# Kernel tuning notes

Hardware: AMD Instinct MI355X
Metric: run time of the kernel (lower is better)

The kernel has to match this reference:

```python
import jax, jax.numpy as jnp
import numpy as np

N = 50000      # num nodes
E = 800000     # num edges (avg degree 16)
D_IN = 128     # input feature dim
H = 128        # hidden dim
RD = 32        # relation embedding dim
L = 2          # num layers
R = 16         # num relations


def setup_inputs() -> dict:
    key = jax.random.key(0)
    ks = jax.random.split(key, 16)
    f32 = jnp.float32
    def lin(k, out_d, in_d):
        return jax.random.normal(k, (out_d, in_d), dtype=f32) * (1.0 / np.sqrt(in_d))
    return {
        "x": jax.random.normal(ks[0], (N, D_IN), dtype=f32),
        "in_W": lin(ks[1], H, D_IN),
        "in_b": jnp.zeros((H,), f32),
        # per-layer stacked params [L, ...]
        "rel_emb": jax.random.normal(ks[2], (L, R, RD), dtype=f32) * 0.02,
        "msg_W": jax.random.normal(ks[3], (L, H, H + RD), dtype=f32) * (1.0 / np.sqrt(H + RD)),
        "msg_b": jnp.zeros((L, H), f32),
        "self_W": jax.random.normal(ks[4], (L, H, H), dtype=f32) * (1.0 / np.sqrt(H)),
        "self_b": jnp.zeros((L, H), f32),
        "neigh_W": jax.random.normal(ks[5], (L, H, H), dtype=f32) * (1.0 / np.sqrt(H)),
        "neigh_b": jnp.zeros((L, H), f32),
        "edge_src": jax.random.randint(ks[6], (E,), 0, N),
        "edge_dst": jax.random.randint(ks[7], (E,), 0, N),
        "rel_ids": jax.random.randint(ks[8], (E,), 0, R),
    }


def reference(x, in_W, in_b, rel_emb, msg_W, msg_b, self_W, self_b,
              neigh_W, neigh_b, edge_src, edge_dst, rel_ids):
    # input projection (dropout is identity at eval)
    h = x @ in_W.T + in_b
    ones_e = jnp.ones((edge_dst.shape[0], 1), h.dtype)
    deg = jax.ops.segment_sum(ones_e, edge_dst, num_segments=N)   # [N,1]
    deg = jnp.maximum(deg, 1.0)
    for l in range(L):
        rel = rel_emb[l][rel_ids]                                  # [E,RD] gather
        msg_in = jnp.concatenate([h[edge_src], rel], axis=-1)      # [E,H+RD]
        msg = msg_in @ msg_W[l].T + msg_b[l]                       # [E,H]
        agg = jax.ops.segment_sum(msg, edge_dst, num_segments=N) / deg  # mean agg
        h = jax.nn.relu(h @ self_W[l].T + self_b[l] + agg @ neigh_W[l].T + neigh_b[l])
    return h
```

## Files before the change

### kernel.cpp

```cpp
#include <hip/hip_runtime.h>
#include <hip/hip_bf16.h>

#define NN 50000
#define EE 800000
#define DH 128
#define RDIM 32
#define RR 16
#define HRD 160
#define HSW 384
#define SCAN_B ((NN + 255) / 256)

typedef __attribute__((ext_vector_type(8))) short bf16x8;
typedef __attribute__((ext_vector_type(4))) float f32x4;

__device__ __forceinline__ ushort f2b(float v) {
    uint u = __float_as_uint(v);
    return (ushort)((u + 0x7fffu + ((u >> 16) & 1u)) >> 16);
}
__device__ __forceinline__ float b2f(ushort b) { return __uint_as_float(((uint)b) << 16); }

__global__ __launch_bounds__(256) void k_count(const int* __restrict__ dst,
                                               int* deg, int* ord) {
    int e = blockIdx.x * 256 + threadIdx.x;
    if (e < EE) ord[e] = atomicAdd(&deg[dst[e]], 1);
}

__global__ __launch_bounds__(256) void k_scan_part(const int* __restrict__ deg,
                                                   int* rp, int* bsum) {
    __shared__ int s[256];
    int tid = threadIdx.x;
    int i = blockIdx.x * 256 + tid;
    int v = (i < NN) ? deg[i] : 0;
    s[tid] = v;
    __syncthreads();
    for (int off = 1; off < 256; off <<= 1) {
        int t = (tid >= off) ? s[tid - off] : 0;
        __syncthreads();
        s[tid] += t;
        __syncthreads();
    }
    if (i < NN) rp[i] = s[tid] - v;
    if (tid == 255) bsum[blockIdx.x] = s[255];
}

__global__ __launch_bounds__(256) void k_scan_bsum(const int* __restrict__ bsum, int* boff) {
    __shared__ int s[256];
    int tid = threadIdx.x;
    int v = (tid < SCAN_B) ? bsum[tid] : 0;
    s[tid] = v;
    __syncthreads();
    for (int off = 1; off < 256; off <<= 1) {
        int t = (tid >= off) ? s[tid - off] : 0;
        __syncthreads();
        s[tid] += t;
        __syncthreads();
    }
    boff[tid] = s[tid] - v;
}

__global__ __launch_bounds__(256) void k_scan_add(const int* __restrict__ boff, int* rp) {
    int i = blockIdx.x * 256 + threadIdx.x;
    if (i < NN) rp[i] += boff[blockIdx.x];
    if (i == 0) rp[NN] = EE;
}

__global__ __launch_bounds__(256) void k_fill(const int* __restrict__ src,
                                              const int* __restrict__ dst,
                                              const int* __restrict__ rel,
                                              const int* __restrict__ ord,
                                              const int* __restrict__ rp,
                                              int* __restrict__ col) {
    int e = blockIdx.x * 256 + threadIdx.x;
    if (e < EE) {
        int p = rp[dst[e]] + ord[e];
        col[p] = src[e] | (rel[e] << 16);
    }
}


__global__ __launch_bounds__(256) void k_prep_inWb(const float* __restrict__ w,
                                                   ushort* __restrict__ o) {
    int i = blockIdx.x * 256 + threadIdx.x;
    o[i] = f2b(w[i]);
}

__global__ __launch_bounds__(256) void k_prep_msgWb(const float* __restrict__ msgW,
                                                    const float* __restrict__ relE,
                                                    ushort* __restrict__ B1,
                                                    float* __restrict__ RMf32) {
    int t = threadIdx.x;
    int l = t >> 7, f = t & 127;
    const float* mw = msgW + (size_t)l * DH * HRD + f * HRD;
    ushort* out = B1 + ((size_t)l * DH + f) * DH;
    for (int k = 0; k < DH; ++k) out[k] = f2b(mw[k]);
    for (int r = 0; r < RR; ++r) {
        float acc = 0.f;
        for (int c = 0; c < RDIM; ++c)
            acc += relE[l * RR * RDIM + r * RDIM + c] * mw[DH + c];
        RMf32[(size_t)l * RR * DH + r * DH + f] = acc;
    }
}

__global__ __launch_bounds__(256) void k_prep_wc2b(const float* __restrict__ selfW,
                                                   const float* __restrict__ neighW,
                                                   ushort* __restrict__ o) {
    int idx = blockIdx.x * 256 + threadIdx.x;
    int l = idx >> 15, rem = idx & 32767;
    int f = rem >> 8, k = rem & 255;
    float v = (k < DH) ? selfW[(size_t)l * DH * DH + f * DH + k]
                       : neighW[(size_t)l * DH * DH + f * DH + (k - DH)];
    o[idx] = f2b(v);
}

__global__ __launch_bounds__(256) void k_seg(ushort* __restrict__ hs,
                                             const int* __restrict__ rp,
                                             const int* __restrict__ col,
                                             const float* __restrict__ RM) {
    __shared__ float RM_s[RR * DH];
    int t = threadIdx.x;
    for (int i = t; i < RR * DH; i += 256) RM_s[i] = RM[i];
    __syncthreads();
    int wid = t >> 6, lane = t & 63;
    int n = blockIdx.x * 4 + wid;
    if (n >= NN) return;
    int beg = rp[n], end = rp[n + 1];
    float ax = 0.f, ay = 0.f, rx = 0.f, ry = 0.f;
    const float* rm0 = RM_s + lane * 2;
    for (int j0 = beg; j0 < end; j0 += 64) {
        int myc = (j0 + lane < end) ? col[j0 + lane] : 0;
        int m = min(64, end - j0);
        for (int jj = 0; jj < m; ++jj) {
            int packed = __shfl(myc, jj, 64);
            int sidx = packed & 0xffff;
            int rel = packed >> 16;
            uint v = *(const uint*)(hs + (size_t)sidx * HSW + lane * 2);
            ax += b2f((ushort)(v & 0xffffu));
            ay += b2f((ushort)(v >> 16));
            rx += rm0[rel * DH];
            ry += rm0[rel * DH + 1];
        }
    }
    uint ps = ((uint)f2b(ay) << 16) | (uint)f2b(ax);
    uint pr = ((uint)f2b(ry) << 16) | (uint)f2b(rx);
    *(uint*)(hs + (size_t)n * HSW + 128 + lane * 2) = ps;
    *(uint*)(hs + (size_t)n * HSW + 256 + lane * 2) = pr;
}

template <int K, int EPI, int AMODE>
__global__ __launch_bounds__(256) void k_mm(const void* __restrict__ Araw,
                                            const ushort* __restrict__ B,
                                            const float* __restrict__ bias1,
                                            const float* __restrict__ bias2,
                                            const int* __restrict__ deg,
                                            ushort* __restrict__ hs,
                                            float* __restrict__ outf) {
    constexpr int KC = (K == 256) ? 128 : K;
    constexpr int NCH = K / KC;
    constexpr int KP = KC + 8;
    __shared__ ushort A_s[64][KP];
    __shared__ ushort B_s[128][KP];
    __shared__ int deg_s[64];
    int t = threadIdx.x;
    int n0 = blockIdx.x * 64;
    int lane = t & 63, wid = t >> 6;
    int wm = wid >> 1, wn = wid & 1;

    if (EPI == 1 && t < 64) {
        int node = n0 + t;
        deg_s[t] = (node < NN) ? deg[node] : 1;
    }

    f32x4 acc[2][4];
    #pragma unroll
    for (int mt = 0; mt < 2; ++mt)
        #pragma unroll
        for (int nt = 0; nt < 4; ++nt) acc[mt][nt] = (f32x4)0.0f;

    for (int ch = 0; ch < NCH; ++ch) {
        int kc0 = ch * KC;
        if (AMODE == 0) {
            const float4* x4 = (const float4*)Araw;
            for (int idx = t; idx < 64 * (KC / 4); idx += 256) {
                int r = idx / (KC / 4), c = idx % (KC / 4);
                int node = min(n0 + r, NN - 1);
                float4 v = x4[(size_t)node * 32 + c];
                ushort* dstp = &A_s[r][c * 4];
                dstp[0] = f2b(v.x); dstp[1] = f2b(v.y);
                dstp[2] = f2b(v.z); dstp[3] = f2b(v.w);
            }
        } else {
            const ushort* Ab = (const ushort*)Araw;
            for (int idx = t; idx < 64 * (KC / 8); idx += 256) {
                int r = idx / (KC / 8), c = idx % (KC / 8);
                int node = min(n0 + r, NN - 1);
                *(uint4*)&A_s[r][c * 8] =
                    *(const uint4*)(Ab + (size_t)node * HSW + kc0 + c * 8);
            }
        }
        for (int idx = t; idx < 128 * (KC / 8); idx += 256) {
            int r = idx / (KC / 8), c = idx % (KC / 8);
            *(uint4*)&B_s[r][c * 8] =
                *(const uint4*)(B + (size_t)r * K + kc0 + c * 8);
        }
        __syncthreads();

        #pragma unroll
        for (int ks = 0; ks < KC / 32; ++ks) {
            int k0 = ks * 32 + (lane >> 4) * 8;
            bf16x8 af[2], bfr[4];
            #pragma unroll
            for (int mt = 0; mt < 2; ++mt)
                af[mt] = *(const bf16x8*)&A_s[wm * 32 + mt * 16 + (lane & 15)][k0];
            #pragma unroll
            for (int nt = 0; nt < 4; ++nt)
                bfr[nt] = *(const bf16x8*)&B_s[wn * 64 + nt * 16 + (lane & 15)][k0];
            #pragma unroll
            for (int mt = 0; mt < 2; ++mt)
                #pragma unroll
                for (int nt = 0; nt < 4; ++nt)
                    acc[mt][nt] = __builtin_amdgcn_mfma_f32_16x16x32_bf16(
                        af[mt], bfr[nt], acc[mt][nt], 0, 0, 0);
        }
        if (ch + 1 < NCH) __syncthreads();
    }

    int fbase = wn * 64;
    #pragma unroll
    for (int mt = 0; mt < 2; ++mt) {
        #pragma unroll
        for (int rg = 0; rg < 4; ++rg) {
            int nl = wm * 32 + mt * 16 + ((lane >> 4) << 2) + rg;
            int node = n0 + nl;
            if (node >= NN) continue;
            #pragma unroll
            for (int nt = 0; nt < 4; ++nt) {
                int f = fbase + nt * 16 + (lane & 15);
                float v = acc[mt][nt][rg];
                if (EPI == 0) {
                    hs[(size_t)node * HSW + f] = f2b(v + bias1[f]);
                } else if (EPI == 1) {
                    int d = deg_s[nl];
                    float rmacc = b2f(hs[(size_t)node * HSW + 256 + f]);
                    float o = (v + rmacc) * (1.f / (float)max(d, 1))
                              + ((d > 0) ? bias1[f] : 0.f);
                    hs[(size_t)node * HSW + 128 + f] = f2b(o);
                } else {
                    float o = fmaxf(v + bias1[f] + bias2[f], 0.f);
                    if (EPI == 2) hs[(size_t)node * HSW + f] = f2b(o);
                    else          outf[(size_t)node * DH + f] = o;
                }
            }
        }
    }
}

extern "C" void kernel_launch(void* const* d_in, const int* in_sizes, int n_in,
                              void* d_out, int out_size, void* d_ws, size_t ws_size,
                              hipStream_t stream) {
    const float* x      = (const float*)d_in[0];
    const float* in_W   = (const float*)d_in[1];
    const float* in_b   = (const float*)d_in[2];
    const float* rel_e  = (const float*)d_in[3];
    const float* msg_W  = (const float*)d_in[4];
    const float* msg_b  = (const float*)d_in[5];
    const float* self_W = (const float*)d_in[6];
    const float* self_b = (const float*)d_in[7];
    const float* neigh_W= (const float*)d_in[8];
    const float* neigh_b= (const float*)d_in[9];
    const int* e_src    = (const int*)d_in[10];
    const int* e_dst    = (const int*)d_in[11];
    const int* r_ids    = (const int*)d_in[12];

    char* ws = (char*)d_ws;
    size_t off = 0;
    ushort* HS   = (ushort*)(ws + off); off += (size_t)NN * HSW * 2;
    ushort* inWb = (ushort*)(ws + off); off += (size_t)DH * DH * 2;
    ushort* B1   = (ushort*)(ws + off); off += 2 * (size_t)DH * DH * 2;
    ushort* Wc2b = (ushort*)(ws + off); off += 2 * (size_t)DH * 256 * 2;
    float*  RMf  = (float*)(ws + off);  off += 2 * (size_t)RR * DH * 4;
    int* deg  = (int*)(ws + off);
    int* rp   = deg + NN;
    int* bsum = rp + NN + 1;
    int* boff = bsum + 256;
    int* ord  = boff + 256;
    int* col  = ord + EE;

    hipMemsetAsync(deg, 0, sizeof(int) * NN, stream);

    k_count<<<(EE + 255) / 256, 256, 0, stream>>>(e_dst, deg, ord);
    k_scan_part<<<SCAN_B, 256, 0, stream>>>(deg, rp, bsum);
    k_scan_bsum<<<1, 256, 0, stream>>>(bsum, boff);
    k_scan_add<<<SCAN_B, 256, 0, stream>>>(boff, rp);
    k_fill<<<(EE + 255) / 256, 256, 0, stream>>>(e_src, e_dst, r_ids, ord, rp, col);

    k_prep_inWb<<<64, 256, 0, stream>>>(in_W, inWb);
    k_prep_msgWb<<<1, 256, 0, stream>>>(msg_W, rel_e, B1, RMf);
    k_prep_wc2b<<<256, 256, 0, stream>>>(self_W, neigh_W, Wc2b);

    const int GB = (NN + 63) / 64;
    k_mm<128, 0, 0><<<GB, 256, 0, stream>>>(x, inWb, in_b, nullptr, nullptr, HS, nullptr);

    for (int l = 0; l < 2; ++l) {
        k_seg<<<(NN + 3) / 4, 256, 0, stream>>>(HS, rp, col, RMf + (size_t)l * RR * DH);
        k_mm<128, 1, 1><<<GB, 256, 0, stream>>>(HS + 128, B1 + (size_t)l * DH * DH,
                                                msg_b + l * DH, nullptr, deg, HS, nullptr);
        if (l == 0)
            k_mm<256, 2, 1><<<GB, 256, 0, stream>>>(HS, Wc2b, self_b, neigh_b,
                                                    nullptr, HS, nullptr);
        else
            k_mm<256, 3, 1><<<GB, 256, 0, stream>>>(HS, Wc2b + (size_t)DH * 256,
                                                    self_b + DH, neigh_b + DH,
                                                    nullptr, HS, (float*)d_out);
    }
}
```

Before: 395.3 us.

## Process four edges per wave in segment aggregation with 16-byte row loads

The segment-sum kernel now splits each 64-lane wave into four groups of 16 lanes. Each group handles a different edge and loads a 16-byte chunk of the bf16 source row instead of a 4-byte pair per lane. Partial sums are combined across the groups with xor shuffles, and only the first group writes the result. The relation-message table is transposed to a [feature][relation] layout so each lane can index it with a stride. The intent is more memory-level parallelism and wider loads in the gather-bound aggregation. The cost is more registers and extra shuffle reductions, and the transposed table may cause LDS bank conflicts.

Measured after the change: 501.3 us. 1.27x slower.

```diff
diff --git a/kernel.cpp b/kernel.cpp
--- a/kernel.cpp
+++ b/kernel.cpp
@@ -77,7 +77,6 @@
     }
 }
 
-
 __global__ __launch_bounds__(256) void k_prep_inWb(const float* __restrict__ w,
                                                    ushort* __restrict__ o) {
     int i = blockIdx.x * 256 + threadIdx.x;
@@ -87,7 +86,7 @@
 __global__ __launch_bounds__(256) void k_prep_msgWb(const float* __restrict__ msgW,
                                                     const float* __restrict__ relE,
                                                     ushort* __restrict__ B1,
-                                                    float* __restrict__ RMf32) {
+                                                    float* __restrict__ RMt) {
     int t = threadIdx.x;
     int l = t >> 7, f = t & 127;
     const float* mw = msgW + (size_t)l * DH * HRD + f * HRD;
@@ -97,7 +96,7 @@
         float acc = 0.f;
         for (int c = 0; c < RDIM; ++c)
             acc += relE[l * RR * RDIM + r * RDIM + c] * mw[DH + c];
-        RMf32[(size_t)l * RR * DH + r * DH + f] = acc;
+        RMt[(size_t)l * DH * RR + f * RR + r] = acc;
     }
 }
 
@@ -115,35 +114,56 @@
 __global__ __launch_bounds__(256) void k_seg(ushort* __restrict__ hs,
                                              const int* __restrict__ rp,
                                              const int* __restrict__ col,
-                                             const float* __restrict__ RM) {
-    __shared__ float RM_s[RR * DH];
+                                             const float* __restrict__ RMt) {
+    __shared__ float RM_s[DH * RR];
     int t = threadIdx.x;
-    for (int i = t; i < RR * DH; i += 256) RM_s[i] = RM[i];
+    for (int i = t; i < DH * RR; i += 256) RM_s[i] = RMt[i];
     __syncthreads();
     int wid = t >> 6, lane = t & 63;
     int n = blockIdx.x * 4 + wid;
     if (n >= NN) return;
     int beg = rp[n], end = rp[n + 1];
-    float ax = 0.f, ay = 0.f, rx = 0.f, ry = 0.f;
-    const float* rm0 = RM_s + lane * 2;
+    int q = lane >> 4, r = lane & 15;
+    float a[8], rm[8];
+    #pragma unroll
+    for (int i = 0; i < 8; ++i) { a[i] = 0.f; rm[i] = 0.f; }
     for (int j0 = beg; j0 < end; j0 += 64) {
         int myc = (j0 + lane < end) ? col[j0 + lane] : 0;
-        int m = min(64, end - j0);
-        for (int jj = 0; jj < m; ++jj) {
-            int packed = __shfl(myc, jj, 64);
-            int sidx = packed & 0xffff;
-            int rel = packed >> 16;
-            uint v = *(const uint*)(hs + (size_t)sidx * HSW + lane * 2);
-            ax += b2f((ushort)(v & 0xffffu));
-            ay += b2f((ushort)(v >> 16));
-            rx += rm0[rel * DH];
-            ry += rm0[rel * DH + 1];
-        }
-    }
-    uint ps = ((uint)f2b(ay) << 16) | (uint)f2b(ax);
-    uint pr = ((uint)f2b(ry) << 16) | (uint)f2b(rx);
-    *(uint*)(hs + (size_t)n * HSW + 128 + lane * 2) = ps;
-    *(uint*)(hs + (size_t)n * HSW + 256 + lane * 2) = pr;
+        int mm = min(end - j0, 64);
+        #pragma unroll 4
+        for (int jj = 0; jj * 4 < mm; ++jj) {
+            int idx = jj * 4 + q;
+            int packed = __shfl(myc, idx, 64);
+            if (idx < mm) {
+                int sidx = packed & 0xffff;
+                int rel = (packed >> 16) & 15;
+                uint4 v = *(const uint4*)(hs + (size_t)sidx * HSW + r * 8);
+                const ushort* pv = (const ushort*)&v;
+                const float* rmp = RM_s + (r * 8) * RR + rel;
+                #pragma unroll
+                for (int i = 0; i < 8; ++i) {
+                    a[i] += b2f(pv[i]);
+                    rm[i] += rmp[i * RR];
+                }
+            }
+        }
+    }
+    #pragma unroll
+    for (int i = 0; i < 8; ++i) {
+        a[i] += __shfl_xor(a[i], 16, 64);  a[i] += __shfl_xor(a[i], 32, 64);
+        rm[i] += __shfl_xor(rm[i], 16, 64); rm[i] += __shfl_xor(rm[i], 32, 64);
+    }
+    if (q == 0) {
+        uint4 W, R;
+        uint* pw = (uint*)&W; uint* pr2 = (uint*)&R;
+        #pragma unroll
+        for (int i = 0; i < 4; ++i) {
+            pw[i]  = (uint)f2b(a[2 * i])  | ((uint)f2b(a[2 * i + 1]) << 16);
+            pr2[i] = (uint)f2b(rm[2 * i]) | ((uint)f2b(rm[2 * i + 1]) << 16);
+        }
+        *(uint4*)(hs + (size_t)n * HSW + 128 + r * 8) = W;
+        *(uint4*)(hs + (size_t)n * HSW + 256 + r * 8) = R;
+    }
 }
 
 template <int K, int EPI, int AMODE>
@@ -277,7 +297,7 @@
     ushort* inWb = (ushort*)(ws + off); off += (size_t)DH * DH * 2;
     ushort* B1   = (ushort*)(ws + off); off += 2 * (size_t)DH * DH * 2;
     ushort* Wc2b = (ushort*)(ws + off); off += 2 * (size_t)DH * 256 * 2;
-    float*  RMf  = (float*)(ws + off);  off += 2 * (size_t)RR * DH * 4;
+    float*  RMt  = (float*)(ws + off);  off += 2 * (size_t)DH * RR * 4;
     int* deg  = (int*)(ws + off);
     int* rp   = deg + NN;
     int* bsum = rp + NN + 1;
@@ -294,14 +314,14 @@
     k_fill<<<(EE + 255) / 256, 256, 0, stream>>>(e_src, e_dst, r_ids, ord, rp, col);
 
     k_prep_inWb<<<64, 256, 0, stream>>>(in_W, inWb);
-    k_prep_msgWb<<<1, 256, 0, stream>>>(msg_W, rel_e, B1, RMf);
+    k_prep_msgWb<<<1, 256, 0, stream>>>(msg_W, rel_e, B1, RMt);
     k_prep_wc2b<<<256, 256, 0, stream>>>(self_W, neigh_W, Wc2b);
 
     const int GB = (NN + 63) / 64;
     k_mm<128, 0, 0><<<GB, 256, 0, stream>>>(x, inWb, in_b, nullptr, nullptr, HS, nullptr);
 
     for (int l = 0; l < 2; ++l) {
-        k_seg<<<(NN + 3) / 4, 256, 0, stream>>>(HS, rp, col, RMf + (size_t)l * RR * DH);
+        k_seg<<<(NN + 3) / 4, 256, 0, stream>>>(HS, rp, col, RMt + (size_t)l * DH * RR);
         k_mm<128, 1, 1><<<GB, 256, 0, stream>>>(HS + 128, B1 + (size_t)l * DH * DH,
                                                 msg_b + l * DH, nullptr, deg, HS, nullptr);
         if (l == 0)
```
